# Kernel tuning notes

Hardware: AMD Instinct MI355X
Metric: run time of the kernel (lower is better)

## Reference

```python
import jax, jax.numpy as jnp
import numpy as np

N, E, IN_C, HID, OUT_C = 50000, 800000, 128, 32, 32
EPS_BN = 1e-5


def gat_layer(x, src, dst, W, a_src, a_dst, bias, heads, out_c, concat):
    n = x.shape[0]
    h = (x @ W).reshape(n, heads, out_c)                    # [N,H,C]
    al_src = jnp.sum(h * a_src, axis=-1)                    # [N,H]
    al_dst = jnp.sum(h * a_dst, axis=-1)                    # [N,H]
    e = jax.nn.leaky_relu(al_src[src] + al_dst[dst], 0.2)   # [Etot,H]
    # segment softmax over incoming edges of each dst node
    m = jax.ops.segment_max(e, dst, num_segments=n)
    e = jnp.exp(e - jax.lax.stop_gradient(m)[dst])
    s = jax.ops.segment_sum(e, dst, num_segments=n)
    alpha = e / (s[dst] + 1e-16)                            # [Etot,H]
    msg = h[src] * alpha[..., None]                         # [Etot,H,C]
    out = jax.ops.segment_sum(msg, dst, num_segments=n)     # [N,H,C]
    out = out.reshape(n, heads * out_c) if concat else out.mean(axis=1)
    return out + bias


def bn_eval(x, w, b, m, v):
    return (x - m) * (w * jax.lax.rsqrt(v + EPS_BN)) + b


def setup_inputs() -> dict:
    key = jax.random.key(0)
    ks = jax.random.split(key, 12)
    f32 = jnp.float32
    inp = {
        'x': jax.random.normal(ks[0], (N, IN_C), dtype=f32),
        'edge_index': jax.random.randint(ks[1], (2, E), 0, N, dtype=jnp.int64),
        'w1': jax.random.normal(ks[2], (IN_C, 4 * HID), dtype=f32) * 0.1,
        'as1': jax.random.normal(ks[3], (4, HID), dtype=f32) * 0.1,
        'ad1': jax.random.normal(ks[4], (4, HID), dtype=f32) * 0.1,
        'b1': jnp.zeros((4 * HID,), f32),
        'bn1_w': jnp.ones((4 * HID,), f32), 'bn1_b': jnp.zeros((4 * HID,), f32),
        'bn1_m': jnp.zeros((4 * HID,), f32), 'bn1_v': jnp.ones((4 * HID,), f32),
        'w2': jax.random.normal(ks[5], (4 * HID, 4 * HID), dtype=f32) * 0.1,
        'as2': jax.random.normal(ks[6], (4, HID), dtype=f32) * 0.1,
        'ad2': jax.random.normal(ks[7], (4, HID), dtype=f32) * 0.1,
        'b2': jnp.zeros((4 * HID,), f32),
        'bn2_w': jnp.ones((4 * HID,), f32), 'bn2_b': jnp.zeros((4 * HID,), f32),
        'bn2_m': jnp.zeros((4 * HID,), f32), 'bn2_v': jnp.ones((4 * HID,), f32),
        'w3': jax.random.normal(ks[8], (4 * HID, OUT_C), dtype=f32) * 0.1,
        'as3': jax.random.normal(ks[9], (1, OUT_C), dtype=f32) * 0.1,
        'ad3': jax.random.normal(ks[10], (1, OUT_C), dtype=f32) * 0.1,
        'b3': jnp.zeros((OUT_C,), f32),
    }
    return inp


def reference(x, edge_index, w1, as1, ad1, b1, bn1_w, bn1_b, bn1_m, bn1_v,
              w2, as2, ad2, b2, bn2_w, bn2_b, bn2_m, bn2_v,
              w3, as3, ad3, b3):
    n = x.shape[0]
    loop = jnp.arange(n, dtype=edge_index.dtype)
    src = jnp.concatenate([edge_index[0], loop])  # add_self_loops (PyG default)
    dst = jnp.concatenate([edge_index[1], loop])
    # layer 1: GAT(heads=4, concat) -> BN(eval) -> relu (dropout=eval identity)
    h = gat_layer(x, src, dst, w1, as1, ad1, b1, 4, HID, True)
    h = jax.nn.relu(bn_eval(h, bn1_w, bn1_b, bn1_m, bn1_v))
    # layer 2
    h = gat_layer(h, src, dst, w2, as2, ad2, b2, 4, HID, True)
    h = jax.nn.relu(bn_eval(h, bn2_w, bn2_b, bn2_m, bn2_v))
    # layer 3: heads=1, concat=False
    return gat_layer(h, src, dst, w3, as3, ad3, b3, 1, OUT_C, False)
```

## Files before the change

### kernel.cpp

```cpp
#include <hip/hip_runtime.h>
#include <hip/hip_fp16.h>
#include <cstdint>


#define NBCHUNK 128
#define MAXBK 512

typedef _Float16 f16x8 __attribute__((ext_vector_type(8)));
typedef float f32x4 __attribute__((ext_vector_type(4)));

__device__ __forceinline__ float lrelu02(float x) {
  return x > 0.f ? x : 0.2f * x;
}

__device__ __forceinline__ float expw(float x) {
  return __expf(fminf(x, 80.f));
}

__device__ __forceinline__ int detect64(const unsigned* ei) {
  int is64 = 1;
  for (int i = 1; i < 128; i += 2)
    if (ei[i] != 0u) { is64 = 0; break; }
  return is64;
}

__global__ __launch_bounds__(256) void bcount_kernel(const void* __restrict__ ei, int E,
                                                     int* __restrict__ counts,
                                                     int nbk, int chunk) {
  __shared__ int hist[MAXBK];
  __shared__ int sIs64;
  for (int i = threadIdx.x; i < nbk; i += 256) hist[i] = 0;
  if (threadIdx.x == 0) sIs64 = detect64((const unsigned*)ei);
  __syncthreads();
  int lo = blockIdx.x * chunk;
  int hi = lo + chunk; if (hi > E) hi = E;
  const bool is64 = sIs64 != 0;
  for (int e = lo + threadIdx.x; e < hi; e += 256) {
    int d = is64 ? (int)((const long long*)ei)[(size_t)E + e] : ((const int*)ei)[E + e];
    atomicAdd(&hist[d >> 7], 1);
  }
  __syncthreads();
  for (int i = threadIdx.x; i < nbk; i += 256)
    counts[(size_t)blockIdx.x * nbk + i] = hist[i];
}

__global__ void bscanT_kernel(int* __restrict__ counts, int* __restrict__ T, int nbk) {
  int b = blockIdx.x;
  int t = threadIdx.x;
  int lane = t & 63;
  int v = counts[(size_t)t * nbk + b];
  int inc = v;
#pragma unroll
  for (int off = 1; off < 64; off <<= 1) {
    int u = __shfl_up(inc, off);
    if (lane >= off) inc += u;
  }
  __shared__ int w0;
  if (t == 63) w0 = inc;
  __syncthreads();
  int wb = (t >= 64) ? w0 : 0;
  counts[(size_t)t * nbk + b] = wb + inc - v;
  if (t == 127) T[b] = wb + inc;
}

__global__ void bscanE_kernel(const int* __restrict__ T, int* __restrict__ EB, int nbk) {
  int lane = threadIdx.x;
  int carry = 0;
  for (int start = 0; start < nbk; start += 64) {
    int i = start + lane;
    int v = (i < nbk) ? T[i] : 0;
    int inc = v;
#pragma unroll
    for (int off = 1; off < 64; off <<= 1) {
      int u = __shfl_up(inc, off);
      if (lane >= off) inc += u;
    }
    if (i < nbk) EB[i] = inc - v + carry;
    carry += __shfl(inc, 63);
  }
  if (lane == 0) EB[nbk] = carry;
}

__global__ __launch_bounds__(256) void bemit_kernel(const void* __restrict__ ei, int E,
                                                    const int* __restrict__ counts,
                                                    const int* __restrict__ EB,
                                                    int nbk, int chunk,
                                                    unsigned* __restrict__ binned) {
  __shared__ int cur[MAXBK];
  __shared__ int sIs64;
  for (int i = threadIdx.x; i < nbk; i += 256)
    cur[i] = counts[(size_t)blockIdx.x * nbk + i] + EB[i];
  if (threadIdx.x == 0) sIs64 = detect64((const unsigned*)ei);
  __syncthreads();
  int lo = blockIdx.x * chunk;
  int hi = lo + chunk; if (hi > E) hi = E;
  const bool is64 = sIs64 != 0;
  for (int e = lo + threadIdx.x; e < hi; e += 256) {
    int s, d;
    if (is64) {
      const long long* p = (const long long*)ei;
      s = (int)p[e];
      d = (int)p[(size_t)E + e];
    } else {
      const int* p = (const int*)ei;
      s = p[e];
      d = p[E + e];
    }
    int pos = atomicAdd(&cur[d >> 7], 1);
    binned[pos] = ((unsigned)(d & 127) << 16) | (unsigned)s;
  }
}

__global__ __launch_bounds__(256) void bscatter2_kernel(const unsigned* __restrict__ binned,
                                                        const int* __restrict__ EB,
                                                        int* __restrict__ row_ptr,
                                                        int* __restrict__ csr_src,
                                                        int n, int E) {
  __shared__ int hist[128];
  __shared__ int cur[128];
  __shared__ int w0s;
  const int b = blockIdx.x;
  const int t = threadIdx.x;
  const int bb = b << 7;
  if (t < 128) hist[t] = 0;
  __syncthreads();
  const int lo = EB[b], hi = EB[b + 1];
  for (int i = lo + t; i < hi; i += 256)
    atomicAdd(&hist[binned[i] >> 16], 1);
  __syncthreads();
  int lane = t & 63;
  int v = (t < 128) ? hist[t] : 0;
  int inc = v;
#pragma unroll
  for (int off = 1; off < 64; off <<= 1) {
    int u = __shfl_up(inc, off);
    if (lane >= off) inc += u;
  }
  if (t == 63) w0s = inc;
  __syncthreads();
  int exc = ((t >= 64 && t < 128) ? w0s : 0) + inc - v;
  if (t < 128 && bb + t < n) {
    int rp = EB[b] + bb + t + exc;
    row_ptr[bb + t] = rp;
    csr_src[rp] = bb + t;
    cur[t] = rp + 1;
  }
  if (b == 0 && t == 0) row_ptr[n] = E + n;
  __syncthreads();
  for (int i = lo + t; i < hi; i += 256) {
    unsigned pv = binned[i];
    int pos = atomicAdd(&cur[pv >> 16], 1);
    csr_src[pos] = (int)(pv & 0xFFFFu);
  }
}

__global__ void wcvt_all_kernel(const float* __restrict__ W1, const float* __restrict__ W2,
                                const float* __restrict__ W3,
                                _Float16* __restrict__ Wt1, _Float16* __restrict__ Wt2,
                                _Float16* __restrict__ Wt3) {
  int idx = blockIdx.x * 256 + threadIdx.x;
  if (idx < 16384) {
    int k = idx >> 7, c = idx & 127;
    Wt1[(size_t)c * 128 + k] = (_Float16)W1[idx];
  } else if (idx < 32768) {
    int i = idx - 16384;
    int k = i >> 7, c = i & 127;
    Wt2[(size_t)c * 128 + k] = (_Float16)W2[i];
  } else if (idx < 36864) {
    int i = idx - 32768;
    int k = i >> 5, c = i & 31;
    Wt3[(size_t)c * 128 + k] = (_Float16)W3[i];
  }
}

template <int OUTC, int H, typename AT>
__global__ __launch_bounds__(256) void mfma_gemm_al_kernel(
    const AT* __restrict__ A, const _Float16* __restrict__ Wt,
    const float* __restrict__ a_src, const float* __restrict__ a_dst,
    __half* __restrict__ Hout, float* __restrict__ alS, float* __restrict__ alD,
    int n) {
  constexpr int NT = OUTC / 16;
  constexpr int APH = 136;

  __shared__ __align__(16) _Float16 A_lds[64 * APH];
  __shared__ __align__(16) _Float16 W_lds[OUTC * APH];

  const int t = threadIdx.x;
  const int r0 = blockIdx.x * 64;

  if constexpr (sizeof(AT) == 4) {
#pragma unroll
    for (int i = 0; i < 8; ++i) {
      int slot = t + i * 256;
      int r = slot >> 5, q = slot & 31;
      float4 v = make_float4(0.f, 0.f, 0.f, 0.f);
      if (r0 + r < n) v = *(const float4*)((const float*)A + (size_t)(r0 + r) * 128 + q * 4);
      __half2 p0 = __floats2half2_rn(v.x, v.y);
      __half2 p1 = __floats2half2_rn(v.z, v.w);
      uint2 pk;
      pk.x = *(unsigned*)&p0;
      pk.y = *(unsigned*)&p1;
      *(uint2*)&A_lds[r * APH + q * 4] = pk;
    }
  } else {
#pragma unroll
    for (int i = 0; i < 4; ++i) {
      int slot = t + i * 256;
      int r = slot >> 4, q = slot & 15;
      uint4 raw = make_uint4(0u, 0u, 0u, 0u);
      if (r0 + r < n) raw = *(const uint4*)((const __half*)A + (size_t)(r0 + r) * 128 + q * 8);
      *(uint4*)&A_lds[r * APH + q * 8] = raw;
    }
  }
#pragma unroll
  for (int i = 0; i < OUTC / 16; ++i) {
    int slot = t + i * 256;
    int c = slot >> 4, q = slot & 15;
    uint4 raw = *(const uint4*)(Wt + (size_t)c * 128 + q * 8);
    *(uint4*)&W_lds[c * APH + q * 8] = raw;
  }
  __syncthreads();

  const int w = t >> 6;
  const int lane = t & 63;
  const int lrow = lane & 15;
  const int lk = lane >> 4;

  f32x4 acc[NT];
#pragma unroll
  for (int i = 0; i < NT; ++i) acc[i] = (f32x4){0.f, 0.f, 0.f, 0.f};

#pragma unroll
  for (int kc = 0; kc < 4; ++kc) {
    f16x8 a = *(const f16x8*)&A_lds[(w * 16 + lrow) * APH + kc * 32 + lk * 8];
#pragma unroll
    for (int ct = 0; ct < NT; ++ct) {
      f16x8 b = *(const f16x8*)&W_lds[(ct * 16 + lrow) * APH + kc * 32 + lk * 8];
      acc[ct] = __builtin_amdgcn_mfma_f32_16x16x32_f16(a, b, acc[ct], 0, 0, 0);
    }
  }

  const int rbase = r0 + w * 16 + lk * 4;
#pragma unroll
  for (int ct = 0; ct < NT; ++ct) {
#pragma unroll
    for (int j = 0; j < 4; ++j) {
      int r = rbase + j;
      if (r < n) Hout[(size_t)r * OUTC + ct * 16 + lrow] = __float2half(acc[ct][j]);
    }
  }

#pragma unroll
  for (int h = 0; h < H; ++h) {
    float as0 = a_src[h * 32 + lrow], as1 = a_src[h * 32 + 16 + lrow];
    float ad0 = a_dst[h * 32 + lrow], ad1 = a_dst[h * 32 + 16 + lrow];
#pragma unroll
    for (int j = 0; j < 4; ++j) {
      float ps = acc[2 * h][j] * as0 + acc[2 * h + 1][j] * as1;
      float pd = acc[2 * h][j] * ad0 + acc[2 * h + 1][j] * ad1;
#pragma unroll
      for (int off = 1; off < 16; off <<= 1) {
        ps += __shfl_xor(ps, off);
        pd += __shfl_xor(pd, off);
      }
      if (lrow == 0) {
        int r = rbase + j;
        if (r < n) {
          alS[(size_t)r * H + h] = ps;
          alD[(size_t)r * H + h] = pd;
        }
      }
    }
  }
}

template <int H, bool BN, typename OutT>
__global__ __launch_bounds__(256) void agg_kernel(
    const int* __restrict__ row_ptr, const int* __restrict__ csr_src,
    const float* __restrict__ alS, const float* __restrict__ alD,
    const __half* __restrict__ hfeat, const float* __restrict__ bias,
    const float* __restrict__ bnw, const float* __restrict__ bnb,
    const float* __restrict__ bnm, const float* __restrict__ bnv,
    OutT* __restrict__ out, int n) {
  constexpr int LPN = (H == 4) ? 64 : 32;
  constexpr int NPB = 256 / LPN;
  constexpr int KCAP = 96;
  constexpr int RSH = (H == 4) ? 8 : 6;

  __shared__ __align__(16) float sW[NPB][KCAP * H];
  __shared__ int sOff[NPB][KCAP];

  const int slot = threadIdx.x / LPN;
  const int sl = threadIdx.x % LPN;
  const int v = blockIdx.x * NPB + slot;
  const bool active = v < n;
  const char* hb = (const char*)hfeat;

  int rs = 0, re = 0;
  if (active) { rs = row_ptr[v]; re = row_ptr[v + 1]; }
  const int deg = re - rs;
  const int degS = deg < KCAP ? deg : KCAP;

  if constexpr (H == 4) {
    float4 ad4 = make_float4(0.f, 0.f, 0.f, 0.f);
    if (active) ad4 = *(const float4*)(alD + (size_t)v * 4);
    float den0 = 0.f, den1 = 0.f, den2 = 0.f, den3 = 0.f;
    for (int k = sl; k < degS; k += 64) {
      int s = csr_src[rs + k];
      sOff[slot][k] = s << RSH;
      float4 a4 = *(const float4*)(alS + (size_t)s * 4);
      float u0 = expw(lrelu02(a4.x + ad4.x));
      float u1 = expw(lrelu02(a4.y + ad4.y));
      float u2 = expw(lrelu02(a4.z + ad4.z));
      float u3 = expw(lrelu02(a4.w + ad4.w));
      ((float4*)&sW[slot][0])[k] = make_float4(u0, u1, u2, u3);
      den0 += u0; den1 += u1; den2 += u2; den3 += u3;
    }
#pragma unroll
    for (int off = 32; off >= 1; off >>= 1) {
      den0 += __shfl_xor(den0, off);
      den1 += __shfl_xor(den1, off);
      den2 += __shfl_xor(den2, off);
      den3 += __shfl_xor(den3, off);
    }

    const int half = sl >> 5;
    const int l5 = sl & 31;
    const int c = l5 * 4;
    const int h = l5 >> 3;
    const unsigned cb2 = (unsigned)(c * 2);
    float a0 = 0.f, a1 = 0.f, a2 = 0.f, a3 = 0.f;
    int j = 0;
    for (; j + 8 <= degS; j += 8) {
      int e0 = j + half, e1 = j + 2 + half, e2 = j + 4 + half, e3 = j + 6 + half;
      unsigned o0 = (unsigned)sOff[slot][e0] + cb2;
      unsigned o1 = (unsigned)sOff[slot][e1] + cb2;
      unsigned o2 = (unsigned)sOff[slot][e2] + cb2;
      unsigned o3 = (unsigned)sOff[slot][e3] + cb2;
      float w0 = sW[slot][e0 * 4 + h], w1 = sW[slot][e1 * 4 + h];
      float w2 = sW[slot][e2 * 4 + h], w3 = sW[slot][e3 * 4 + h];
      uint2 r0v = *(const uint2*)(hb + o0);
      uint2 r1v = *(const uint2*)(hb + o1);
      uint2 r2v = *(const uint2*)(hb + o2);
      uint2 r3v = *(const uint2*)(hb + o3);
      float2 f0l = __half22float2(*(const __half2*)&r0v.x);
      float2 f0h = __half22float2(*(const __half2*)&r0v.y);
      float2 f1l = __half22float2(*(const __half2*)&r1v.x);
      float2 f1h = __half22float2(*(const __half2*)&r1v.y);
      float2 f2l = __half22float2(*(const __half2*)&r2v.x);
      float2 f2h = __half22float2(*(const __half2*)&r2v.y);
      float2 f3l = __half22float2(*(const __half2*)&r3v.x);
      float2 f3h = __half22float2(*(const __half2*)&r3v.y);
      a0 = fmaf(w0, f0l.x, a0); a1 = fmaf(w0, f0l.y, a1);
      a2 = fmaf(w0, f0h.x, a2); a3 = fmaf(w0, f0h.y, a3);
      a0 = fmaf(w1, f1l.x, a0); a1 = fmaf(w1, f1l.y, a1);
      a2 = fmaf(w1, f1h.x, a2); a3 = fmaf(w1, f1h.y, a3);
      a0 = fmaf(w2, f2l.x, a0); a1 = fmaf(w2, f2l.y, a1);
      a2 = fmaf(w2, f2h.x, a2); a3 = fmaf(w2, f2h.y, a3);
      a0 = fmaf(w3, f3l.x, a0); a1 = fmaf(w3, f3l.y, a1);
      a2 = fmaf(w3, f3h.x, a2); a3 = fmaf(w3, f3h.y, a3);
    }
    for (; j + 2 <= degS; j += 2) {
      int e = j + half;
      unsigned o = (unsigned)sOff[slot][e] + cb2;
      float w = sW[slot][e * 4 + h];
      uint2 rv = *(const uint2*)(hb + o);
      float2 fl = __half22float2(*(const __half2*)&rv.x);
      float2 fh = __half22float2(*(const __half2*)&rv.y);
      a0 = fmaf(w, fl.x, a0); a1 = fmaf(w, fl.y, a1);
      a2 = fmaf(w, fh.x, a2); a3 = fmaf(w, fh.y, a3);
    }
    if ((degS & 1) && half == 0) {
      int e = degS - 1;
      unsigned o = (unsigned)sOff[slot][e] + cb2;
      float w = sW[slot][e * 4 + h];
      uint2 rv = *(const uint2*)(hb + o);
      float2 fl = __half22float2(*(const __half2*)&rv.x);
      float2 fh = __half22float2(*(const __half2*)&rv.y);
      a0 = fmaf(w, fl.x, a0); a1 = fmaf(w, fl.y, a1);
      a2 = fmaf(w, fh.x, a2); a3 = fmaf(w, fh.y, a3);
    }
    a0 += __shfl_xor(a0, 32);
    a1 += __shfl_xor(a1, 32);
    a2 += __shfl_xor(a2, 32);
    a3 += __shfl_xor(a3, 32);

    float den = (h == 0) ? den0 : (h == 1) ? den1 : (h == 2) ? den2 : den3;
    if (deg > KCAP) {
      float adh = alD[(size_t)v * 4 + h];
      if (half == 0) {
        for (int e = rs + KCAP; e < re; ++e) {
          int s = csr_src[e];
          float u = expw(lrelu02(alS[(size_t)s * 4 + h] + adh));
          den += u;
          uint2 rv = *(const uint2*)(hb + ((unsigned)(s << RSH) + cb2));
          float2 fl = __half22float2(*(const __half2*)&rv.x);
          float2 fh = __half22float2(*(const __half2*)&rv.y);
          a0 = fmaf(u, fl.x, a0); a1 = fmaf(u, fl.y, a1);
          a2 = fmaf(u, fh.x, a2); a3 = fmaf(u, fh.y, a3);
        }
      } else {
        for (int e = rs + KCAP; e < re; ++e) {
          int s = csr_src[e];
          den += expw(lrelu02(alS[(size_t)s * 4 + h] + adh));
        }
      }
    }
    if (active && half == 0) {
      float inv = 1.f / (den + 1e-16f);
      float4 b4 = *(const float4*)(bias + c);
      float g0 = a0 * inv + b4.x;
      float g1 = a1 * inv + b4.y;
      float g2 = a2 * inv + b4.z;
      float g3 = a3 * inv + b4.w;
      if constexpr (BN) {
        float4 bw = *(const float4*)(bnw + c);
        float4 bb = *(const float4*)(bnb + c);
        float4 bm = *(const float4*)(bnm + c);
        float4 bv = *(const float4*)(bnv + c);
        g0 = fmaxf((g0 - bm.x) * (bw.x * rsqrtf(bv.x + 1e-5f)) + bb.x, 0.f);
        g1 = fmaxf((g1 - bm.y) * (bw.y * rsqrtf(bv.y + 1e-5f)) + bb.y, 0.f);
        g2 = fmaxf((g2 - bm.z) * (bw.z * rsqrtf(bv.z + 1e-5f)) + bb.z, 0.f);
        g3 = fmaxf((g3 - bm.w) * (bw.w * rsqrtf(bv.w + 1e-5f)) + bb.w, 0.f);
      }
      if constexpr (sizeof(OutT) == 2) {
        __half2 p0 = __floats2half2_rn(g0, g1);
        __half2 p1 = __floats2half2_rn(g2, g3);
        uint2 pk;
        pk.x = *(unsigned*)&p0;
        pk.y = *(unsigned*)&p1;
        *(uint2*)((__half*)out + (size_t)v * 128 + c) = pk;
      } else {
        *(float4*)((float*)out + (size_t)v * 128 + c) = make_float4(g0, g1, g2, g3);
      }
    }
  } else {
    float ad = active ? alD[v] : 0.f;
    float den = 0.f;
    for (int k = sl; k < degS; k += 32) {
      int s = csr_src[rs + k];
      sOff[slot][k] = s << RSH;
      float u = expw(lrelu02(alS[s] + ad));
      sW[slot][k] = u;
      den += u;
    }
#pragma unroll
    for (int off = 16; off >= 1; off >>= 1) den += __shfl_xor(den, off);

    const int quad = sl >> 4;
    const int l4 = sl & 15;
    const int c2 = l4 * 2;
    const unsigned cb2 = (unsigned)(c2 * 2);
    float a0 = 0.f, a1 = 0.f;
    int j = 0;
    for (; j + 4 <= degS; j += 4) {
      int e0 = j + quad, e1 = j + 2 + quad;
      unsigned o0 = (unsigned)sOff[slot][e0] + cb2;
      unsigned o1 = (unsigned)sOff[slot][e1] + cb2;
      float w0 = sW[slot][e0], w1 = sW[slot][e1];
      float2 f0 = __half22float2(*(const __half2*)(hb + o0));
      float2 f1 = __half22float2(*(const __half2*)(hb + o1));
      a0 = fmaf(w0, f0.x, a0); a1 = fmaf(w0, f0.y, a1);
      a0 = fmaf(w1, f1.x, a0); a1 = fmaf(w1, f1.y, a1);
    }
    for (; j + 2 <= degS; j += 2) {
      int e = j + quad;
      unsigned o = (unsigned)sOff[slot][e] + cb2;
      float w = sW[slot][e];
      float2 f = __half22float2(*(const __half2*)(hb + o));
      a0 = fmaf(w, f.x, a0); a1 = fmaf(w, f.y, a1);
    }
    if ((degS & 1) && quad == 0) {
      int e = degS - 1;
      unsigned o = (unsigned)sOff[slot][e] + cb2;
      float w = sW[slot][e];
      float2 f = __half22float2(*(const __half2*)(hb + o));
      a0 = fmaf(w, f.x, a0); a1 = fmaf(w, f.y, a1);
    }
    a0 += __shfl_xor(a0, 16);
    a1 += __shfl_xor(a1, 16);

    if (deg > KCAP) {
      if (quad == 0) {
        for (int e = rs + KCAP; e < re; ++e) {
          int s = csr_src[e];
          float u = expw(lrelu02(alS[s] + ad));
          den += u;
          float2 f = __half22float2(*(const __half2*)(hb + ((unsigned)(s << RSH) + cb2)));
          a0 = fmaf(u, f.x, a0); a1 = fmaf(u, f.y, a1);
        }
      } else {
        for (int e = rs + KCAP; e < re; ++e)
          den += expw(lrelu02(alS[csr_src[e]] + ad));
      }
    }
    if (active && quad == 0) {
      float inv = 1.f / (den + 1e-16f);
      float2 b2v = *(const float2*)(bias + c2);
      ((float2*)((float*)out + (size_t)v * 32))[l4] =
          make_float2(a0 * inv + b2v.x, a1 * inv + b2v.y);
    }
  }
}

extern "C" void kernel_launch(void* const* d_in, const int* in_sizes, int n_in,
                              void* d_out, int out_size, void* d_ws, size_t ws_size,
                              hipStream_t stream) {
  const float* x = (const float*)d_in[0];
  const void* ei = d_in[1];
  const float* w1 = (const float*)d_in[2];
  const float* as1 = (const float*)d_in[3];
  const float* ad1 = (const float*)d_in[4];
  const float* b1 = (const float*)d_in[5];
  const float* bn1w = (const float*)d_in[6];
  const float* bn1b = (const float*)d_in[7];
  const float* bn1m = (const float*)d_in[8];
  const float* bn1v = (const float*)d_in[9];
  const float* w2 = (const float*)d_in[10];
  const float* as2 = (const float*)d_in[11];
  const float* ad2 = (const float*)d_in[12];
  const float* b2 = (const float*)d_in[13];
  const float* bn2w = (const float*)d_in[14];
  const float* bn2b = (const float*)d_in[15];
  const float* bn2m = (const float*)d_in[16];
  const float* bn2v = (const float*)d_in[17];
  const float* w3 = (const float*)d_in[18];
  const float* as3 = (const float*)d_in[19];
  const float* ad3 = (const float*)d_in[20];
  const float* b3 = (const float*)d_in[21];

  const int N = in_sizes[0] / 128;
  const int E = in_sizes[1] / 2;
  const int nbk = (N + 127) / 128;
  const int chunk = (E + NBCHUNK - 1) / NBCHUNK;

  char* base = (char*)d_ws;
  size_t off = 0;
  auto alloc = [&](size_t bytes) {
    void* p = base + off;
    off = (off + bytes + 255) & ~(size_t)255;
    return p;
  };
  int* counts = (int*)alloc((size_t)NBCHUNK * nbk * 4);
  int* T = (int*)alloc((size_t)nbk * 4);
  int* EB = (int*)alloc((size_t)(nbk + 1) * 4);
  unsigned* binned = (unsigned*)alloc((size_t)E * 4);
  int* row_ptr = (int*)alloc((size_t)(N + 1) * 4);
  int* csr_src = (int*)alloc((size_t)(E + N) * 4);
  _Float16* Wt1 = (_Float16*)alloc((size_t)128 * 128 * 2);
  _Float16* Wt2 = (_Float16*)alloc((size_t)128 * 128 * 2);
  _Float16* Wt3 = (_Float16*)alloc((size_t)32 * 128 * 2);
  __half* hbuf = (__half*)alloc((size_t)N * 128 * 2);
  __half* gbuf = (__half*)alloc((size_t)N * 128 * 2);
  float* alS = (float*)alloc((size_t)N * 4 * 4);
  float* alD = (float*)alloc((size_t)N * 4 * 4);
  (void)ws_size;

  wcvt_all_kernel<<<144, 256, 0, stream>>>(w1, w2, w3, Wt1, Wt2, Wt3);
  bcount_kernel<<<NBCHUNK, 256, 0, stream>>>(ei, E, counts, nbk, chunk);
  bscanT_kernel<<<nbk, NBCHUNK, 0, stream>>>(counts, T, nbk);
  bscanE_kernel<<<1, 64, 0, stream>>>(T, EB, nbk);
  bemit_kernel<<<NBCHUNK, 256, 0, stream>>>(ei, E, counts, EB, nbk, chunk, binned);
  bscatter2_kernel<<<nbk, 256, 0, stream>>>(binned, EB, row_ptr, csr_src, N, E);

  const int rowBlocks = (N + 63) / 64;

  mfma_gemm_al_kernel<128, 4, float><<<rowBlocks, 256, 0, stream>>>(
      x, Wt1, as1, ad1, hbuf, alS, alD, N);
  agg_kernel<4, true, __half><<<(N + 3) / 4, 256, 0, stream>>>(
      row_ptr, csr_src, alS, alD, hbuf, b1, bn1w, bn1b, bn1m, bn1v, gbuf, N);
  mfma_gemm_al_kernel<128, 4, __half><<<rowBlocks, 256, 0, stream>>>(
      gbuf, Wt2, as2, ad2, hbuf, alS, alD, N);
  agg_kernel<4, true, __half><<<(N + 3) / 4, 256, 0, stream>>>(
      row_ptr, csr_src, alS, alD, hbuf, b2, bn2w, bn2b, bn2m, bn2v, gbuf, N);
  mfma_gemm_al_kernel<32, 1, __half><<<rowBlocks, 256, 0, stream>>>(
      gbuf, Wt3, as3, ad3, hbuf, alS, alD, N);
  agg_kernel<1, false, float><<<(N + 7) / 8, 256, 0, stream>>>(
      row_ptr, csr_src, alS, alD, hbuf, b3, nullptr, nullptr, nullptr, nullptr,
      (float*)d_out, N);
}
```

Before: 192.0 us.

## Fuse CSR build and weight conversion into one cooperative kernel with grid syncs

Merges the six preprocessing kernels (weight transpose/convert, bucket count, two scans, emit, scatter) into a single cooperative launch separated by grid.sync barriers. Weight conversion runs on extra blocks alongside the bucket counting. The aim is to remove five kernel launch gaps. In exchange it adds grid-wide barrier costs, requires every block of the roughly 391-block grid to be co-resident, and has a single block do the serial scan while the others wait.

```diff
diff --git a/kernel.cpp b/kernel.cpp
--- a/kernel.cpp
+++ b/kernel.cpp
@@ -1,6 +1,9 @@
 #include <hip/hip_runtime.h>
 #include <hip/hip_fp16.h>
+#include <hip/hip_cooperative_groups.h>
 #include <cstdint>
+
+namespace cg = cooperative_groups;
 
 
 #define NBCHUNK 128
@@ -24,152 +27,148 @@
   return is64;
 }
 
-__global__ __launch_bounds__(256) void bcount_kernel(const void* __restrict__ ei, int E,
-                                                     int* __restrict__ counts,
-                                                     int nbk, int chunk) {
-  __shared__ int hist[MAXBK];
-  __shared__ int sIs64;
-  for (int i = threadIdx.x; i < nbk; i += 256) hist[i] = 0;
-  if (threadIdx.x == 0) sIs64 = detect64((const unsigned*)ei);
-  __syncthreads();
-  int lo = blockIdx.x * chunk;
-  int hi = lo + chunk; if (hi > E) hi = E;
-  const bool is64 = sIs64 != 0;
-  for (int e = lo + threadIdx.x; e < hi; e += 256) {
-    int d = is64 ? (int)((const long long*)ei)[(size_t)E + e] : ((const int*)ei)[E + e];
-    atomicAdd(&hist[d >> 7], 1);
-  }
-  __syncthreads();
-  for (int i = threadIdx.x; i < nbk; i += 256)
-    counts[(size_t)blockIdx.x * nbk + i] = hist[i];
-}
-
-__global__ void bscanT_kernel(int* __restrict__ counts, int* __restrict__ T, int nbk) {
-  int b = blockIdx.x;
-  int t = threadIdx.x;
-  int lane = t & 63;
-  int v = counts[(size_t)t * nbk + b];
-  int inc = v;
-#pragma unroll
-  for (int off = 1; off < 64; off <<= 1) {
-    int u = __shfl_up(inc, off);
-    if (lane >= off) inc += u;
-  }
-  __shared__ int w0;
-  if (t == 63) w0 = inc;
-  __syncthreads();
-  int wb = (t >= 64) ? w0 : 0;
-  counts[(size_t)t * nbk + b] = wb + inc - v;
-  if (t == 127) T[b] = wb + inc;
-}
-
-__global__ void bscanE_kernel(const int* __restrict__ T, int* __restrict__ EB, int nbk) {
-  int lane = threadIdx.x;
-  int carry = 0;
-  for (int start = 0; start < nbk; start += 64) {
-    int i = start + lane;
-    int v = (i < nbk) ? T[i] : 0;
+__global__ __launch_bounds__(256) void build_kernel(
+    const void* __restrict__ ei, int E, int n, int nbk, int chunk,
+    const float* __restrict__ W1, const float* __restrict__ W2,
+    const float* __restrict__ W3,
+    _Float16* __restrict__ Wt1, _Float16* __restrict__ Wt2,
+    _Float16* __restrict__ Wt3,
+    int* __restrict__ counts, int* __restrict__ T, int* __restrict__ EB,
+    unsigned* __restrict__ binned, int* __restrict__ row_ptr,
+    int* __restrict__ csr_src) {
+  cg::grid_group grid = cg::this_grid();
+  __shared__ int sH[MAXBK];
+  __shared__ int sC[128];
+  __shared__ int sMisc[2];
+  const int b = blockIdx.x;
+  const int t = threadIdx.x;
+
+  if (b < NBCHUNK) {
+    for (int i = t; i < nbk; i += 256) sH[i] = 0;
+    if (t == 0) sMisc[1] = detect64((const unsigned*)ei);
+    __syncthreads();
+    int lo = b * chunk;
+    int hi = lo + chunk; if (hi > E) hi = E;
+    const bool is64 = sMisc[1] != 0;
+    for (int e = lo + t; e < hi; e += 256) {
+      int d = is64 ? (int)((const long long*)ei)[(size_t)E + e] : ((const int*)ei)[E + e];
+      atomicAdd(&sH[d >> 7], 1);
+    }
+    __syncthreads();
+    for (int i = t; i < nbk; i += 256)
+      counts[(size_t)b * nbk + i] = sH[i];
+  } else {
+    int nOther = gridDim.x - NBCHUNK;
+    for (int idx = (b - NBCHUNK) * 256 + t; idx < 36864; idx += nOther * 256) {
+      if (idx < 16384) {
+        int k = idx >> 7, c = idx & 127;
+        Wt1[(size_t)c * 128 + k] = (_Float16)W1[idx];
+      } else if (idx < 32768) {
+        int i = idx - 16384;
+        int k = i >> 7, c = i & 127;
+        Wt2[(size_t)c * 128 + k] = (_Float16)W2[i];
+      } else {
+        int i = idx - 32768;
+        int k = i >> 5, c = i & 31;
+        Wt3[(size_t)c * 128 + k] = (_Float16)W3[i];
+      }
+    }
+  }
+  grid.sync();
+
+  if (b < nbk) {
+    int lane = t & 63;
+    int v = (t < 128) ? counts[(size_t)t * nbk + b] : 0;
     int inc = v;
 #pragma unroll
     for (int off = 1; off < 64; off <<= 1) {
       int u = __shfl_up(inc, off);
       if (lane >= off) inc += u;
     }
-    if (i < nbk) EB[i] = inc - v + carry;
-    carry += __shfl(inc, 63);
-  }
-  if (lane == 0) EB[nbk] = carry;
-}
-
-__global__ __launch_bounds__(256) void bemit_kernel(const void* __restrict__ ei, int E,
-                                                    const int* __restrict__ counts,
-                                                    const int* __restrict__ EB,
-                                                    int nbk, int chunk,
-                                                    unsigned* __restrict__ binned) {
-  __shared__ int cur[MAXBK];
-  __shared__ int sIs64;
-  for (int i = threadIdx.x; i < nbk; i += 256)
-    cur[i] = counts[(size_t)blockIdx.x * nbk + i] + EB[i];
-  if (threadIdx.x == 0) sIs64 = detect64((const unsigned*)ei);
-  __syncthreads();
-  int lo = blockIdx.x * chunk;
-  int hi = lo + chunk; if (hi > E) hi = E;
-  const bool is64 = sIs64 != 0;
-  for (int e = lo + threadIdx.x; e < hi; e += 256) {
-    int s, d;
-    if (is64) {
-      const long long* p = (const long long*)ei;
-      s = (int)p[e];
-      d = (int)p[(size_t)E + e];
-    } else {
-      const int* p = (const int*)ei;
-      s = p[e];
-      d = p[E + e];
-    }
-    int pos = atomicAdd(&cur[d >> 7], 1);
-    binned[pos] = ((unsigned)(d & 127) << 16) | (unsigned)s;
-  }
-}
-
-__global__ __launch_bounds__(256) void bscatter2_kernel(const unsigned* __restrict__ binned,
-                                                        const int* __restrict__ EB,
-                                                        int* __restrict__ row_ptr,
-                                                        int* __restrict__ csr_src,
-                                                        int n, int E) {
-  __shared__ int hist[128];
-  __shared__ int cur[128];
-  __shared__ int w0s;
-  const int b = blockIdx.x;
-  const int t = threadIdx.x;
-  const int bb = b << 7;
-  if (t < 128) hist[t] = 0;
-  __syncthreads();
-  const int lo = EB[b], hi = EB[b + 1];
-  for (int i = lo + t; i < hi; i += 256)
-    atomicAdd(&hist[binned[i] >> 16], 1);
-  __syncthreads();
-  int lane = t & 63;
-  int v = (t < 128) ? hist[t] : 0;
-  int inc = v;
-#pragma unroll
-  for (int off = 1; off < 64; off <<= 1) {
-    int u = __shfl_up(inc, off);
-    if (lane >= off) inc += u;
-  }
-  if (t == 63) w0s = inc;
-  __syncthreads();
-  int exc = ((t >= 64 && t < 128) ? w0s : 0) + inc - v;
-  if (t < 128 && bb + t < n) {
-    int rp = EB[b] + bb + t + exc;
-    row_ptr[bb + t] = rp;
-    csr_src[rp] = bb + t;
-    cur[t] = rp + 1;
-  }
-  if (b == 0 && t == 0) row_ptr[n] = E + n;
-  __syncthreads();
-  for (int i = lo + t; i < hi; i += 256) {
-    unsigned pv = binned[i];
-    int pos = atomicAdd(&cur[pv >> 16], 1);
-    csr_src[pos] = (int)(pv & 0xFFFFu);
-  }
-}
-
-__global__ void wcvt_all_kernel(const float* __restrict__ W1, const float* __restrict__ W2,
-                                const float* __restrict__ W3,
-                                _Float16* __restrict__ Wt1, _Float16* __restrict__ Wt2,
-                                _Float16* __restrict__ Wt3) {
-  int idx = blockIdx.x * 256 + threadIdx.x;
-  if (idx < 16384) {
-    int k = idx >> 7, c = idx & 127;
-    Wt1[(size_t)c * 128 + k] = (_Float16)W1[idx];
-  } else if (idx < 32768) {
-    int i = idx - 16384;
-    int k = i >> 7, c = i & 127;
-    Wt2[(size_t)c * 128 + k] = (_Float16)W2[i];
-  } else if (idx < 36864) {
-    int i = idx - 32768;
-    int k = i >> 5, c = i & 31;
-    Wt3[(size_t)c * 128 + k] = (_Float16)W3[i];
+    if (t == 63) sMisc[0] = inc;
+    __syncthreads();
+    int wb = (t >= 64 && t < 128) ? sMisc[0] : 0;
+    if (t < 128) counts[(size_t)t * nbk + b] = wb + inc - v;
+    if (t == 127) T[b] = wb + inc;
+  }
+  grid.sync();
+
+  if (b == 0 && t < 64) {
+    int lane = t;
+    int carry = 0;
+    for (int start = 0; start < nbk; start += 64) {
+      int i = start + lane;
+      int v = (i < nbk) ? T[i] : 0;
+      int inc = v;
+#pragma unroll
+      for (int off = 1; off < 64; off <<= 1) {
+        int u = __shfl_up(inc, off);
+        if (lane >= off) inc += u;
+      }
+      if (i < nbk) EB[i] = inc - v + carry;
+      carry += __shfl(inc, 63);
+    }
+    if (lane == 0) EB[nbk] = carry;
+  }
+  grid.sync();
+
+  if (b < NBCHUNK) {
+    for (int i = t; i < nbk; i += 256)
+      sH[i] = counts[(size_t)b * nbk + i] + EB[i];
+    if (t == 0) sMisc[1] = detect64((const unsigned*)ei);
+    __syncthreads();
+    int lo = b * chunk;
+    int hi = lo + chunk; if (hi > E) hi = E;
+    const bool is64 = sMisc[1] != 0;
+    for (int e = lo + t; e < hi; e += 256) {
+      int s, d;
+      if (is64) {
+        const long long* p = (const long long*)ei;
+        s = (int)p[e];
+        d = (int)p[(size_t)E + e];
+      } else {
+        const int* p = (const int*)ei;
+        s = p[e];
+        d = p[E + e];
+      }
+      int pos = atomicAdd(&sH[d >> 7], 1);
+      binned[pos] = ((unsigned)(d & 127) << 16) | (unsigned)s;
+    }
+  }
+  grid.sync();
+
+  if (b < nbk) {
+    const int bb = b << 7;
+    if (t < 128) sH[t] = 0;
+    __syncthreads();
+    const int lo = EB[b], hi = EB[b + 1];
+    for (int i = lo + t; i < hi; i += 256)
+      atomicAdd(&sH[binned[i] >> 16], 1);
+    __syncthreads();
+    int lane = t & 63;
+    int v = (t < 128) ? sH[t] : 0;
+    int inc = v;
+#pragma unroll
+    for (int off = 1; off < 64; off <<= 1) {
+      int u = __shfl_up(inc, off);
+      if (lane >= off) inc += u;
+    }
+    if (t == 63) sMisc[0] = inc;
+    __syncthreads();
+    int exc = ((t >= 64 && t < 128) ? sMisc[0] : 0) + inc - v;
+    if (t < 128 && bb + t < n) {
+      int rp = EB[b] + bb + t + exc;
+      row_ptr[bb + t] = rp;
+      csr_src[rp] = bb + t;
+      sC[t] = rp + 1;
+    }
+    if (b == 0 && t == 0) row_ptr[n] = E + n;
+    __syncthreads();
+    for (int i = lo + t; i < hi; i += 256) {
+      unsigned pv = binned[i];
+      int pos = atomicAdd(&sC[pv >> 16], 1);
+      csr_src[pos] = (int)(pv & 0xFFFFu);
+    }
   }
 }
 
@@ -531,8 +530,9 @@
 
   const int N = in_sizes[0] / 128;
   const int E = in_sizes[1] / 2;
-  const int nbk = (N + 127) / 128;
+  int nbk = (N + 127) / 128;
   const int chunk = (E + NBCHUNK - 1) / NBCHUNK;
+  int buildGrid = nbk > (NBCHUNK + 64) ? nbk : (NBCHUNK + 64);
 
   char* base = (char*)d_ws;
   size_t off = 0;
@@ -556,12 +556,20 @@
   float* alD = (float*)alloc((size_t)N * 4 * 4);
   (void)ws_size;
 
-  wcvt_all_kernel<<<144, 256, 0, stream>>>(w1, w2, w3, Wt1, Wt2, Wt3);
-  bcount_kernel<<<NBCHUNK, 256, 0, stream>>>(ei, E, counts, nbk, chunk);
-  bscanT_kernel<<<nbk, NBCHUNK, 0, stream>>>(counts, T, nbk);
-  bscanE_kernel<<<1, 64, 0, stream>>>(T, EB, nbk);
-  bemit_kernel<<<NBCHUNK, 256, 0, stream>>>(ei, E, counts, EB, nbk, chunk, binned);
-  bscatter2_kernel<<<nbk, 256, 0, stream>>>(binned, EB, row_ptr, csr_src, N, E);
+  {
+    const void* ei_ = ei;
+    int E_ = E, n_ = N, nbk_ = nbk, chunk_ = chunk;
+    const float *W1_ = w1, *W2_ = w2, *W3_ = w3;
+    _Float16 *Wt1_ = Wt1, *Wt2_ = Wt2, *Wt3_ = Wt3;
+    int *counts_ = counts, *T_ = T, *EB_ = EB;
+    unsigned* binned_ = binned;
+    int *row_ptr_ = row_ptr, *csr_src_ = csr_src;
+    void* args[] = {&ei_, &E_, &n_, &nbk_, &chunk_, &W1_, &W2_, &W3_,
+                    &Wt1_, &Wt2_, &Wt3_, &counts_, &T_, &EB_, &binned_,
+                    &row_ptr_, &csr_src_};
+    hipLaunchCooperativeKernel((void*)build_kernel, dim3(buildGrid), dim3(256),
+                               args, 0, stream);
+  }
 
   const int rowBlocks = (N + 63) / 64;
 
```

Measured after the change: 377.7 us. +96.7%, slower.
